# Optimization experiments

Hardware: AMD Instinct MI355X
Metric: run time of the kernel (lower is better)

## Reference

```python
import jax, jax.numpy as jnp
import numpy as np
from jax import lax

B, N, C = 8, 8192, 64
ODR, K, OUT = 4, 32, 128
S = N // ODR
EPS = 1e-5


def _lbr(h, W, b, g, be):
    # h: [M, K, Cin] -> linear -> BN (training-mode batch stats over (M,K) per channel) -> relu
    y = jnp.einsum('mki,oi->mko', h, W) + b
    mean = y.mean(axis=(0, 1))
    var = ((y - mean) ** 2).mean(axis=(0, 1))  # biased var, as torch BN uses for normalization
    y = (y - mean) * lax.rsqrt(var + EPS) * g + be
    return jax.nn.relu(y)


def setup_inputs() -> dict:
    key = jax.random.key(0)
    ks = jax.random.split(key, 12)
    x = jax.random.normal(ks[0], (B, N, C), dtype=jnp.float32)
    coor = jax.random.normal(ks[1], (B, N, 3), dtype=jnp.float32)
    indx = jax.random.permutation(ks[2], N)[:S]  # like torch.randperm(N)[:S]
    w1 = jax.random.normal(ks[3], (OUT, 2 * C), dtype=jnp.float32) * (2 * C) ** -0.5
    b1 = jax.random.normal(ks[4], (OUT,), dtype=jnp.float32) * 0.01
    g1 = jax.random.uniform(ks[5], (OUT,), dtype=jnp.float32, minval=0.5, maxval=1.5)
    be1 = jax.random.normal(ks[6], (OUT,), dtype=jnp.float32) * 0.01
    w2 = jax.random.normal(ks[7], (OUT, OUT), dtype=jnp.float32) * OUT ** -0.5
    b2 = jax.random.normal(ks[8], (OUT,), dtype=jnp.float32) * 0.01
    g2 = jax.random.uniform(ks[9], (OUT,), dtype=jnp.float32, minval=0.5, maxval=1.5)
    be2 = jax.random.normal(ks[10], (OUT,), dtype=jnp.float32) * 0.01
    return dict(x=x, coor=coor, indx=indx, w1=w1, b1=b1, g1=g1, be1=be1,
                w2=w2, b2=b2, g2=g2, be2=be2)


def reference(x, coor, indx, w1, b1, g1, be1, w2, b2, g2, be2):
    sampled_coor = coor[:, indx, :]  # [B,S,3]
    sampled_x = x[:, indx, :]        # [B,S,C]
    # pairwise squared distances [B,S,N]
    dist = jnp.sum((coor[:, None, :, :] - sampled_coor[:, :, None, :]) ** 2, axis=-1)
    # k smallest distances == argsort(dist)[..., :K]
    _, knn_idx = lax.top_k(-dist, K)  # [B,S,K]
    knn_x = jax.vmap(lambda xb, ib: xb[ib])(x, knn_idx)  # [B,S,K,C]
    rep_x = jnp.broadcast_to(sampled_x[:, :, None, :], (x.shape[0], S, K, x.shape[2]))
    feat = jnp.concatenate([rep_x, knn_x - rep_x], axis=-1)  # [B,S,K,2C]
    feat = feat.reshape(x.shape[0] * S, K, 2 * x.shape[2])
    h = _lbr(feat, w1, b1, g1, be1)
    h = _lbr(h, w2, b2, g2, be2)
    h = h.reshape(x.shape[0], S, K, -1)
    out = jnp.max(h, axis=2)  # [B,S,OUT]
    return out, sampled_coor
```

## Files before the change

kernel.cpp:

```cpp
#include <hip/hip_runtime.h>
#include <stdint.h>


#define N_    8192
#define GPB_  8

typedef __attribute__((ext_vector_type(8))) short bf8;
typedef __attribute__((ext_vector_type(16))) float f32x16;

__device__ __forceinline__ unsigned int bf1u(float f) {
  unsigned int u = __float_as_uint(f);
  return (u + 0x7fffu + ((u >> 16) & 1u)) >> 16;
}
__device__ __forceinline__ unsigned int bfpair(float lo, float hi) {
  return bf1u(lo) | (bf1u(hi) << 16);
}

__global__ __launch_bounds__(256) void kprep(const float* __restrict__ w1,
                                             const float* __restrict__ w2,
                                             const float* __restrict__ coor,
                                             const int* __restrict__ indx,
                                             unsigned short* __restrict__ w1b,
                                             unsigned short* __restrict__ w2b,
                                             float* __restrict__ outc,
                                             float4* __restrict__ coor4) {
  int e = blockIdx.x * 256 + threadIdx.x;
  if (e < 16384) {
    w1b[e] = (unsigned short)bf1u(w1[e]);
  } else if (e < 32768) {
    int e2 = e - 16384;
    w2b[e2] = (unsigned short)bf1u(w2[e2]);
  } else if (e < 81920) {
    int e2 = e - 32768;
    int bs = e2 / 3, c = e2 - bs * 3;
    int b = bs >> 11, s = bs & 2047;
    outc[e2] = coor[(b * N_ + indx[s]) * 3 + c];
  } else {
    int p = e - 81920;
    const float* src = coor + (size_t)p * 3;
    coor4[p] = make_float4(src[0], src[1], src[2], 0.f);
  }
}

__global__ __launch_bounds__(256, 8) void kknn(const float4* __restrict__ coor4,
                                               const int* __restrict__ indx,
                                               int* __restrict__ knn) {
  __shared__ float sdist[16 * 256];
  __shared__ float smin[128];
  __shared__ float smrg[64];
  __shared__ float sT;
  __shared__ unsigned long long cands[128];
  __shared__ unsigned long long ssort[128];
  __shared__ int ccnt;

  const int gid = blockIdx.x;
  const int b = gid >> 11, s = gid & 2047;
  const int tid = threadIdx.x;
  const int w = tid >> 6, lane = tid & 63;
  const float4* cb = coor4 + ((size_t)b << 13);
  const float4 q = cb[indx[s]];

  float rdist[16];
  float dmin = 3.4e38f;
#pragma unroll
  for (int it = 0; it < 16; ++it) {
    const float4 c = cb[tid + (it << 8)];
    const float dx = __fsub_rn(c.x, q.x);
    const float dy = __fsub_rn(c.y, q.y);
    const float dz = __fsub_rn(c.z, q.z);
    const float d =
        __fadd_rn(__fadd_rn(__fmul_rn(dx, dx), __fmul_rn(dy, dy)), __fmul_rn(dz, dz));
    rdist[it] = d;
    dmin = fminf(dmin, d);
  }
#pragma unroll 8
  for (int it = 16; it < 32; ++it) {
    const float4 c = cb[tid + (it << 8)];
    const float dx = __fsub_rn(c.x, q.x);
    const float dy = __fsub_rn(c.y, q.y);
    const float dz = __fsub_rn(c.z, q.z);
    const float d =
        __fadd_rn(__fadd_rn(__fmul_rn(dx, dx), __fmul_rn(dy, dy)), __fmul_rn(dz, dz));
    sdist[(it - 16) * 256 + tid] = d;
    dmin = fminf(dmin, d);
  }
  if (tid == 0) ccnt = 0;
  if (tid < 128) cands[tid] = ~0ULL;

  float v = dmin;
#pragma unroll
  for (int k = 2; k <= 64; k <<= 1) {
#pragma unroll
    for (int j = k >> 1; j >= 1; j >>= 1) {
      const float o = __shfl_xor(v, j, 64);
      const bool dirAsc = ((lane & k) == 0);
      const bool lower = ((lane & j) == 0);
      const float lo = fminf(v, o), hi = fmaxf(v, o);
      v = (dirAsc == lower) ? lo : hi;
    }
  }
  if (lane < 32) smin[w * 32 + lane] = v;
  __syncthreads();
  if (w < 2) {
    float a = (lane < 32) ? smin[w * 64 + lane] : smin[w * 64 + 32 + (63 - lane)];
#pragma unroll
    for (int j = 32; j >= 1; j >>= 1) {
      const float o = __shfl_xor(a, j, 64);
      const float lo = fminf(a, o), hi = fmaxf(a, o);
      a = ((lane & j) == 0) ? lo : hi;
    }
    if (lane < 32) smrg[w * 32 + lane] = a;
  }
  __syncthreads();
  if (w == 0) {
    float a = (lane < 32) ? smrg[lane] : smrg[32 + (63 - lane)];
#pragma unroll
    for (int j = 32; j >= 1; j >>= 1) {
      const float o = __shfl_xor(a, j, 64);
      const float lo = fminf(a, o), hi = fmaxf(a, o);
      a = ((lane & j) == 0) ? lo : hi;
    }
    if (lane == 31) sT = a;
  }
  __syncthreads();
  const float T = sT;

#pragma unroll
  for (int it = 0; it < 16; ++it) {
    const float d = rdist[it];
    if (d <= T) {
      const int pos = atomicAdd(&ccnt, 1);
      if (pos < 128)
        cands[pos] = ((unsigned long long)__float_as_uint(d) << 32) |
                     (unsigned int)(tid + (it << 8));
    }
  }
#pragma unroll 8
  for (int it = 16; it < 32; ++it) {
    const float d = sdist[(it - 16) * 256 + tid];
    if (d <= T) {
      const int pos = atomicAdd(&ccnt, 1);
      if (pos < 128)
        cands[pos] = ((unsigned long long)__float_as_uint(d) << 32) |
                     (unsigned int)(tid + (it << 8));
    }
  }
  __syncthreads();

  if (w < 2) {
    unsigned long long kv = cands[w * 64 + lane];
#pragma unroll
    for (int k = 2; k <= 64; k <<= 1) {
#pragma unroll
      for (int j = k >> 1; j >= 1; j >>= 1) {
        const unsigned long long o = __shfl_xor(kv, j, 64);
        const bool dirAsc = ((lane & k) == 0);
        const bool lower = ((lane & j) == 0);
        const unsigned long long lo = o < kv ? o : kv;
        const unsigned long long hi = o < kv ? kv : o;
        kv = (dirAsc == lower) ? lo : hi;
      }
    }
    ssort[w * 64 + lane] = kv;
  }
  __syncthreads();
  if (w == 0) {
    const unsigned long long a = ssort[lane];
    const unsigned long long b2 = ssort[64 + 63 - lane];
    unsigned long long m = a < b2 ? a : b2;
#pragma unroll
    for (int j = 32; j >= 1; j >>= 1) {
      const unsigned long long o = __shfl_xor(m, j, 64);
      const unsigned long long lo = o < m ? o : m;
      const unsigned long long hi = o < m ? m : o;
      m = ((lane & j) == 0) ? lo : hi;
    }
    if (lane < 32) knn[gid * 32 + lane] = (int)(unsigned int)m;
  }
}

template <int PHASE>
__global__ __launch_bounds__(256, 4) void kphase(
    const float* __restrict__ x, const int* __restrict__ indx,
    const int* __restrict__ knn, const float* __restrict__ b1,
    const unsigned short* __restrict__ w1b, const unsigned short* __restrict__ w2b,
    const float* __restrict__ b2, const float* __restrict__ st1,
    float* __restrict__ part, float* __restrict__ mout) {
  __shared__ __align__(16) float sx[64];
  __shared__ __align__(16) unsigned short sxb[72];
  __shared__ __align__(16) unsigned short dls[32 * 68 + 8];
  __shared__ __align__(16) unsigned short h1[PHASE == 2 ? 32 * 136 : 8];

  const int tid = threadIdx.x;
  const int w = tid >> 6;
  const int lane = tid & 63;
  const int m = lane & 31, q2 = lane >> 5;
  const int col = (w << 5) + m;
  const int r8 = tid >> 3, c8 = (tid & 7) * 8;

  const int bb = blockIdx.x & 7;
  const int jj = blockIdx.x >> 3;
  const float* xb = x + (size_t)bb * (N_ * 64);
  const int gidbase = (bb << 11) + jj * GPB_;

  bf8 bf1[8];
#pragma unroll
  for (int t = 0; t < 8; ++t)
    bf1[t] = *(const bf8*)&w1b[col * 128 + t * 16 + q2 * 8];
  bf8 bf2[8];
  float s1 = 0.f, t1 = 0.f, b2v = 0.f;
  if constexpr (PHASE == 2) {
#pragma unroll
    for (int t = 0; t < 8; ++t)
      bf2[t] = *(const bf8*)&w2b[col * 128 + t * 16 + q2 * 8];
    s1 = st1[col];
    t1 = st1[128 + col];
    b2v = b2[col];
  }
  (void)w2b; (void)b2; (void)st1; (void)mout;
  const float b1c = b1[col];

  float sum = 0.f, ssq = 0.f;

  int idxp = indx[jj * GPB_];
  float sxv = (tid < 64) ? xb[(size_t)idxp * 64 + tid] : 0.f;
  int nbr = knn[(size_t)gidbase * 32 + r8];

#pragma unroll 1
  for (int g = 0; g < GPB_; ++g) {
    const int gid = gidbase + g;
    if (tid < 64) sx[tid] = sxv;
    __syncthreads();

    {
      const float* xrow = xb + (size_t)nbr * 64 + c8;
      const float4 xa = *(const float4*)(xrow);
      const float4 xc = *(const float4*)(xrow + 4);
      const float4 sa = *(const float4*)(sx + c8);
      const float4 sc = *(const float4*)(sx + c8 + 4);
      uint2 lo, hi;
      lo.x = bfpair(xa.x - sa.x, xa.y - sa.y);
      lo.y = bfpair(xa.z - sa.z, xa.w - sa.w);
      hi.x = bfpair(xc.x - sc.x, xc.y - sc.y);
      hi.y = bfpair(xc.z - sc.z, xc.w - sc.w);
      *(uint2*)&dls[r8 * 68 + c8] = lo;
      *(uint2*)&dls[r8 * 68 + c8 + 4] = hi;
    }
    if (tid < 16) {
      const float4 sv = *(const float4*)(sx + tid * 4);
      uint2 p;
      p.x = bfpair(sv.x, sv.y);
      p.y = bfpair(sv.z, sv.w);
      *(uint2*)&sxb[tid * 4] = p;
    }

    if (g + 1 < GPB_) {
      const int s1n = jj * GPB_ + g + 1;
      const int idx1 = indx[s1n];
      sxv = (tid < 64) ? xb[(size_t)idx1 * 64 + tid] : 0.f;
      nbr = knn[(size_t)(gid + 1) * 32 + r8];
    }
    __syncthreads();

    bf8 af[8];
#pragma unroll
    for (int t = 0; t < 4; ++t) {
      union { bf8 v; uint2 u[2]; } fa;
      fa.u[0] = *(const uint2*)&sxb[t * 16 + q2 * 8];
      fa.u[1] = *(const uint2*)&sxb[t * 16 + q2 * 8 + 4];
      af[t] = fa.v;
    }
#pragma unroll
    for (int t = 0; t < 4; ++t) {
      union { bf8 v; uint2 u[2]; } fa;
      fa.u[0] = *(const uint2*)&dls[m * 68 + t * 16 + q2 * 8];
      fa.u[1] = *(const uint2*)&dls[m * 68 + t * 16 + q2 * 8 + 4];
      af[4 + t] = fa.v;
    }

    f32x16 acc;
#pragma unroll
    for (int r = 0; r < 16; ++r) acc[r] = b1c;
#pragma unroll
    for (int t = 0; t < 8; ++t)
      acc = __builtin_amdgcn_mfma_f32_32x32x16_bf16(af[t], bf1[t], acc, 0, 0, 0);

    if constexpr (PHASE == 1) {
#pragma unroll
      for (int r = 0; r < 16; ++r) {
        const float v = acc[r];
        sum += v;
        ssq = fmaf(v, v, ssq);
      }
    } else {
#pragma unroll
      for (int r = 0; r < 16; ++r) {
        const float hv = fmaxf(0.f, fmaf(acc[r], s1, t1));
        const int row = (r & 3) + ((r >> 2) << 3) + (q2 << 2);
        h1[row * 136 + col] = (unsigned short)bf1u(hv);
      }
      __syncthreads();

      f32x16 acc2;
#pragma unroll
      for (int r = 0; r < 16; ++r) acc2[r] = b2v;
#pragma unroll
      for (int t = 0; t < 8; ++t) {
        const bf8 a2 = *(const bf8*)&h1[m * 136 + t * 16 + q2 * 8];
        acc2 = __builtin_amdgcn_mfma_f32_32x32x16_bf16(a2, bf2[t], acc2, 0, 0, 0);
      }

      float mx = -1e30f;
#pragma unroll
      for (int r = 0; r < 16; ++r) {
        const float v = acc2[r];
        sum += v;
        ssq = fmaf(v, v, ssq);
        mx = fmaxf(mx, v);
      }
      mx = fmaxf(mx, __shfl_xor(mx, 32, 64));
      if (lane < 32) mout[(size_t)gid * 128 + col] = mx;
    }
  }

  sum += __shfl_xor(sum, 32, 64);
  ssq += __shfl_xor(ssq, 32, 64);
  if (lane < 32) {
    part[blockIdx.x * 256 + col] = sum;
    part[blockIdx.x * 256 + 128 + col] = ssq;
  }
}

__global__ __launch_bounds__(256) void kred1(const float* __restrict__ part,
                                             double* __restrict__ dbuf) {
  const int blk = blockIdx.x;
  const int c = threadIdx.x;
  const float* p = part + (size_t)blk * 32 * 256 + c;
  double acc = 0.0;
#pragma unroll 8
  for (int r = 0; r < 32; ++r) acc += (double)p[r * 256];
  dbuf[blk * 256 + c] = acc;
}

__global__ __launch_bounds__(256) void kred2(const double* __restrict__ dbuf,
                                             const float* __restrict__ gam,
                                             const float* __restrict__ bet,
                                             float* __restrict__ st) {
  __shared__ double sS[256];
  const int c = threadIdx.x;
  double acc = 0.0;
#pragma unroll 8
  for (int i = 0; i < 64; ++i) acc += dbuf[i * 256 + c];
  sS[c] = acc;
  __syncthreads();
  if (c < 128) {
    const double Sv = sS[c], SSv = sS[128 + c];
    const double cnt = 524288.0;
    const double mean = Sv / cnt;
    const double var = SSv / cnt - mean * mean;
    const double scale = (double)gam[c] / sqrt(var + 1e-5);
    st[c] = (float)scale;
    st[128 + c] = (float)((double)bet[c] - mean * scale);
  }
}

__global__ __launch_bounds__(256) void kout(const float* __restrict__ m,
                                            const float* __restrict__ st2,
                                            float* __restrict__ out) {
  const int e4 = blockIdx.x * 256 + threadIdx.x;
  const int o0 = (e4 & 31) * 4;
  const float4 v = ((const float4*)m)[e4];
  const float4 sc = *(const float4*)&st2[o0];
  const float4 sh = *(const float4*)&st2[128 + o0];
  float4 r;
  r.x = fmaxf(0.f, fmaf(v.x, sc.x, sh.x));
  r.y = fmaxf(0.f, fmaf(v.y, sc.y, sh.y));
  r.z = fmaxf(0.f, fmaf(v.z, sc.z, sh.z));
  r.w = fmaxf(0.f, fmaf(v.w, sc.w, sh.w));
  ((float4*)out)[e4] = r;
}

extern "C" void kernel_launch(void* const* d_in, const int* in_sizes, int n_in,
                              void* d_out, int out_size, void* d_ws, size_t ws_size,
                              hipStream_t stream) {
  (void)in_sizes; (void)n_in; (void)out_size; (void)ws_size;
  const float* x    = (const float*)d_in[0];
  const float* coor = (const float*)d_in[1];
  const int*   indx = (const int*)d_in[2];
  const float* w1   = (const float*)d_in[3];
  const float* b1   = (const float*)d_in[4];
  const float* g1   = (const float*)d_in[5];
  const float* be1  = (const float*)d_in[6];
  const float* w2   = (const float*)d_in[7];
  const float* b2   = (const float*)d_in[8];
  const float* g2   = (const float*)d_in[9];
  const float* be2  = (const float*)d_in[10];
  float* out = (float*)d_out;

  char* ws = (char*)d_ws;
  int*            knn   = (int*)(ws + 0);
  float*          mbuf  = (float*)(ws + 2097152);
  float*          part1 = (float*)(ws + 10485760);
  float4*         coor4 = (float4*)(ws + 10485760);
  float*          part2 = (float*)(ws + 12582912);
  unsigned short* w1b   = (unsigned short*)(ws + 14680064);
  unsigned short* w2b   = (unsigned short*)(ws + 14712832);
  float*          st1   = (float*)(ws + 14745600);
  float*          st2   = (float*)(ws + 14746624);
  double*         dbuf  = (double*)(ws + 14747648);

  float* outc = out + 2097152;

  kprep<<<576, 256, 0, stream>>>(w1, w2, coor, indx, w1b, w2b, outc, coor4);
  kknn<<<16384, 256, 0, stream>>>(coor4, indx, knn);
  kphase<1><<<2048, 256, 0, stream>>>(x, indx, knn, b1, w1b, w2b, b2, nullptr,
                                      part1, nullptr);
  kred1<<<64, 256, 0, stream>>>(part1, dbuf);
  kred2<<<1, 256, 0, stream>>>(dbuf, g1, be1, st1);
  kphase<2><<<2048, 256, 0, stream>>>(x, indx, knn, b1, w1b, w2b, b2, st1,
                                      part2, mbuf);
  kred1<<<64, 256, 0, stream>>>(part2, dbuf);
  kred2<<<1, 256, 0, stream>>>(dbuf, g2, be2, st2);
  kout<<<2048, 256, 0, stream>>>(mbuf, st2, out);
}
```

Before: 288.4 us.

## Use SoA coordinates and packed FP32 math in KNN distance computation

The prep kernel now stores the coordinates as separate X/Y/Z arrays instead of padded float4 records. The KNN kernel reads four points per thread with float4 loads and computes squared distances with v_pk_add/v_pk_mul packed FP32 instructions. It also spills half of the distances to shared memory as float4 rather than scalars. This should cut wasted load bandwidth on the padding and halve the VALU instruction count for the distance stage. Each thread now owns contiguous points, which changes the candidate index mapping and the order in which ties are inserted.

After: 289.9 us. No clear change (+0.5%).

```diff
diff --git a/kernel.cpp b/kernel.cpp
--- a/kernel.cpp
+++ b/kernel.cpp
@@ -7,6 +7,7 @@
 
 typedef __attribute__((ext_vector_type(8))) short bf8;
 typedef __attribute__((ext_vector_type(16))) float f32x16;
+typedef __attribute__((ext_vector_type(2))) float f32x2;
 
 __device__ __forceinline__ unsigned int bf1u(float f) {
   unsigned int u = __float_as_uint(f);
@@ -14,6 +15,17 @@
 }
 __device__ __forceinline__ unsigned int bfpair(float lo, float hi) {
   return bf1u(lo) | (bf1u(hi) << 16);
+}
+
+__device__ __forceinline__ f32x2 pk_add(f32x2 a, f32x2 b) {
+  f32x2 d;
+  asm("v_pk_add_f32 %0, %1, %2" : "=v"(d) : "v"(a), "v"(b));
+  return d;
+}
+__device__ __forceinline__ f32x2 pk_mul(f32x2 a, f32x2 b) {
+  f32x2 d;
+  asm("v_pk_mul_f32 %0, %1, %2" : "=v"(d) : "v"(a), "v"(b));
+  return d;
 }
 
 __global__ __launch_bounds__(256) void kprep(const float* __restrict__ w1,
@@ -23,7 +35,7 @@
                                              unsigned short* __restrict__ w1b,
                                              unsigned short* __restrict__ w2b,
                                              float* __restrict__ outc,
-                                             float4* __restrict__ coor4) {
+                                             float* __restrict__ soa) {
   int e = blockIdx.x * 256 + threadIdx.x;
   if (e < 16384) {
     w1b[e] = (unsigned short)bf1u(w1[e]);
@@ -37,15 +49,19 @@
     outc[e2] = coor[(b * N_ + indx[s]) * 3 + c];
   } else {
     int p = e - 81920;
+    const int b = p >> 13, i = p & 8191;
     const float* src = coor + (size_t)p * 3;
-    coor4[p] = make_float4(src[0], src[1], src[2], 0.f);
-  }
-}
-
-__global__ __launch_bounds__(256, 8) void kknn(const float4* __restrict__ coor4,
+    float* dst = soa + b * 24576;
+    dst[i]         = src[0];
+    dst[8192 + i]  = src[1];
+    dst[16384 + i] = src[2];
+  }
+}
+
+__global__ __launch_bounds__(256, 8) void kknn(const float* __restrict__ soa,
                                                const int* __restrict__ indx,
                                                int* __restrict__ knn) {
-  __shared__ float sdist[16 * 256];
+  __shared__ __align__(16) float4 sdist4[4 * 256];
   __shared__ float smin[128];
   __shared__ float smrg[64];
   __shared__ float sT;
@@ -57,33 +73,45 @@
   const int b = gid >> 11, s = gid & 2047;
   const int tid = threadIdx.x;
   const int w = tid >> 6, lane = tid & 63;
-  const float4* cb = coor4 + ((size_t)b << 13);
-  const float4 q = cb[indx[s]];
-
-  float rdist[16];
-  float dmin = 3.4e38f;
-#pragma unroll
-  for (int it = 0; it < 16; ++it) {
-    const float4 c = cb[tid + (it << 8)];
-    const float dx = __fsub_rn(c.x, q.x);
-    const float dy = __fsub_rn(c.y, q.y);
-    const float dz = __fsub_rn(c.z, q.z);
-    const float d =
-        __fadd_rn(__fadd_rn(__fmul_rn(dx, dx), __fmul_rn(dy, dy)), __fmul_rn(dz, dz));
-    rdist[it] = d;
-    dmin = fminf(dmin, d);
-  }
-#pragma unroll 8
-  for (int it = 16; it < 32; ++it) {
-    const float4 c = cb[tid + (it << 8)];
-    const float dx = __fsub_rn(c.x, q.x);
-    const float dy = __fsub_rn(c.y, q.y);
-    const float dz = __fsub_rn(c.z, q.z);
-    const float d =
-        __fadd_rn(__fadd_rn(__fmul_rn(dx, dx), __fmul_rn(dy, dy)), __fmul_rn(dz, dz));
-    sdist[(it - 16) * 256 + tid] = d;
-    dmin = fminf(dmin, d);
-  }
+  const float* Xb = soa + b * 24576;
+  const float* Yb = Xb + 8192;
+  const float* Zb = Xb + 16384;
+  const int qi = indx[s];
+  const float qx = Xb[qi], qy = Yb[qi], qz = Zb[qi];
+  const f32x2 nqx = {-qx, -qx}, nqy = {-qy, -qy}, nqz = {-qz, -qz};
+
+  f32x2 rd[8];
+  f32x2 dmL = {3.4e38f, 3.4e38f}, dmH = {3.4e38f, 3.4e38f};
+#pragma unroll
+  for (int it = 0; it < 8; ++it) {
+    const int ofs = (it << 10) + (tid << 2);
+    union { float4 f4; f32x2 h[2]; } X, Y, Z;
+    X.f4 = *(const float4*)(Xb + ofs);
+    Y.f4 = *(const float4*)(Yb + ofs);
+    Z.f4 = *(const float4*)(Zb + ofs);
+    const f32x2 dxl = pk_add(X.h[0], nqx), dyl = pk_add(Y.h[0], nqy),
+                dzl = pk_add(Z.h[0], nqz);
+    const f32x2 dxh = pk_add(X.h[1], nqx), dyh = pk_add(Y.h[1], nqy),
+                dzh = pk_add(Z.h[1], nqz);
+    const f32x2 sl =
+        pk_add(pk_add(pk_mul(dxl, dxl), pk_mul(dyl, dyl)), pk_mul(dzl, dzl));
+    const f32x2 sh =
+        pk_add(pk_add(pk_mul(dxh, dxh), pk_mul(dyh, dyh)), pk_mul(dzh, dzh));
+    dmL.x = fminf(dmL.x, sl.x);
+    dmL.y = fminf(dmL.y, sl.y);
+    dmH.x = fminf(dmH.x, sh.x);
+    dmH.y = fminf(dmH.y, sh.y);
+    if (it < 4) {
+      rd[it * 2] = sl;
+      rd[it * 2 + 1] = sh;
+    } else {
+      union { float4 f4; f32x2 h[2]; } st;
+      st.h[0] = sl;
+      st.h[1] = sh;
+      sdist4[((it - 4) << 8) + tid] = st.f4;
+    }
+  }
+  float dmin = fminf(fminf(dmL.x, dmL.y), fminf(dmH.x, dmH.y));
   if (tid == 0) ccnt = 0;
   if (tid < 128) cands[tid] = ~0ULL;
 
@@ -126,23 +154,35 @@
   const float T = sT;
 
 #pragma unroll
-  for (int it = 0; it < 16; ++it) {
-    const float d = rdist[it];
-    if (d <= T) {
+  for (int t = 0; t < 8; ++t) {
+    const int p0 = ((t >> 1) << 10) + (tid << 2) + ((t & 1) << 1);
+    const float d0 = rd[t].x, d1 = rd[t].y;
+    if (d0 <= T) {
       const int pos = atomicAdd(&ccnt, 1);
       if (pos < 128)
-        cands[pos] = ((unsigned long long)__float_as_uint(d) << 32) |
-                     (unsigned int)(tid + (it << 8));
-    }
-  }
-#pragma unroll 8
-  for (int it = 16; it < 32; ++it) {
-    const float d = sdist[(it - 16) * 256 + tid];
-    if (d <= T) {
+        cands[pos] = ((unsigned long long)__float_as_uint(d0) << 32) |
+                     (unsigned int)p0;
+    }
+    if (d1 <= T) {
       const int pos = atomicAdd(&ccnt, 1);
       if (pos < 128)
-        cands[pos] = ((unsigned long long)__float_as_uint(d) << 32) |
-                     (unsigned int)(tid + (it << 8));
+        cands[pos] = ((unsigned long long)__float_as_uint(d1) << 32) |
+                     (unsigned int)(p0 + 1);
+    }
+  }
+#pragma unroll
+  for (int it = 4; it < 8; ++it) {
+    const float4 d4 = sdist4[((it - 4) << 8) + tid];
+    const int p0 = (it << 10) + (tid << 2);
+    const float dd[4] = {d4.x, d4.y, d4.z, d4.w};
+#pragma unroll
+    for (int j = 0; j < 4; ++j) {
+      if (dd[j] <= T) {
+        const int pos = atomicAdd(&ccnt, 1);
+        if (pos < 128)
+          cands[pos] = ((unsigned long long)__float_as_uint(dd[j]) << 32) |
+                       (unsigned int)(p0 + j);
+      }
     }
   }
   __syncthreads();
@@ -401,7 +441,7 @@
   int*            knn   = (int*)(ws + 0);
   float*          mbuf  = (float*)(ws + 2097152);
   float*          part1 = (float*)(ws + 10485760);
-  float4*         coor4 = (float4*)(ws + 10485760);
+  float*          soa   = (float*)(ws + 10485760);
   float*          part2 = (float*)(ws + 12582912);
   unsigned short* w1b   = (unsigned short*)(ws + 14680064);
   unsigned short* w2b   = (unsigned short*)(ws + 14712832);
@@ -411,8 +451,8 @@
 
   float* outc = out + 2097152;
 
-  kprep<<<576, 256, 0, stream>>>(w1, w2, coor, indx, w1b, w2b, outc, coor4);
-  kknn<<<16384, 256, 0, stream>>>(coor4, indx, knn);
+  kprep<<<576, 256, 0, stream>>>(w1, w2, coor, indx, w1b, w2b, outc, soa);
+  kknn<<<16384, 256, 0, stream>>>(soa, indx, knn);
   kphase<1><<<2048, 256, 0, stream>>>(x, indx, knn, b1, w1b, w2b, b2, nullptr,
                                       part1, nullptr);
   kred1<<<64, 256, 0, stream>>>(part1, dbuf);
```
